# Performance work log

Hardware: AMD Instinct MI355X
Metric: run time of the kernel (lower is better)

Reference implementation:

```python
import jax, jax.numpy as jnp
import numpy as np

INPUT_SIZE = 512
N_THETA = 608  # backcast 512 + forecast 96
N_EXPERTS = 8
TOP_K = 2
LN_EPS = 1e-5


def setup_inputs() -> dict:
    key = jax.random.key(0)
    ks = jax.random.split(key, 5)
    B = 8192
    s = 0.02
    return {
        "insample_y": jax.random.normal(ks[0], (B, INPUT_SIZE), dtype=jnp.float32),
        "ln_gamma": jnp.ones((INPUT_SIZE,), dtype=jnp.float32),
        "ln_beta": jnp.zeros((INPUT_SIZE,), dtype=jnp.float32),
        "Wg": jax.random.normal(ks[1], (INPUT_SIZE, N_EXPERTS), dtype=jnp.float32) * s,
        "W0": jax.random.normal(ks[2], (N_EXPERTS, INPUT_SIZE, 512), dtype=jnp.float32) * s,
        "Wmid": jax.random.normal(ks[3], (3, N_EXPERTS, 512, 512), dtype=jnp.float32) * s,
        "Wout": jax.random.normal(ks[4], (N_EXPERTS, 512, N_THETA), dtype=jnp.float32) * s,
    }


def _layer_norm(x, gamma, beta):
    mu = jnp.mean(x, axis=-1, keepdims=True)
    var = jnp.mean(jnp.square(x - mu), axis=-1, keepdims=True)
    return (x - mu) * jax.lax.rsqrt(var + LN_EPS) * gamma + beta


def reference(insample_y, ln_gamma, ln_beta, Wg, W0, Wmid, Wout):
    x = insample_y  # [B, input_size]
    # Gate: LayerNorm -> Linear(no bias) -> top-k -> softmax over selected logits
    gate_logits = _layer_norm(x, ln_gamma, ln_beta) @ Wg            # [B, E]
    top_vals, top_idx = jax.lax.top_k(gate_logits, TOP_K)           # [B, k]
    gate_w = jax.nn.softmax(top_vals, axis=-1)                      # [B, k]

    # Experts (bias-free MLPs), evaluated densely for all experts
    z = jnp.einsum('bi,eih->beh', x, W0)                            # first linear, no activation
    for l in range(Wmid.shape[0]):
        z = jax.nn.relu(jnp.einsum('beh,eho->beo', z, Wmid[l]))
    theta_all = jnp.einsum('beh,eht->bet', z, Wout)                 # [B, E, n_theta]

    # Combine top-k expert outputs with gate weights
    theta_sel = jnp.take_along_axis(theta_all, top_idx[:, :, None], axis=1)  # [B, k, n_theta]
    theta = jnp.einsum('bk,bkt->bt', gate_w, theta_sel)             # [B, n_theta]

    # Identity basis: split theta into backcast / forecast
    backcast = theta[:, :INPUT_SIZE]
    forecast = theta[:, INPUT_SIZE:]
    return backcast, forecast
```

## Files before the change

kernel.cpp:

```cpp
#include <hip/hip_runtime.h>
#include <hip/hip_bf16.h>
#include <stdint.h>


#define B_ROWS 8192
#define I_DIM  512
#define H_DIM  512
#define E_NUM  8
#define T_DIM  608
#define T_PAD  640
#define CAP    2304
#define TPE    18
#define NT     144
#define NPAD   18432

typedef unsigned short ushort_t;
typedef __attribute__((ext_vector_type(8))) __bf16 bf16x8;
typedef __attribute__((ext_vector_type(8))) unsigned short ushort8;
typedef __attribute__((ext_vector_type(4))) float floatx4;

__device__ __forceinline__ void gload_lds16(const void* g, void* l) {
  __builtin_amdgcn_global_load_lds(
      (const __attribute__((address_space(1))) unsigned int*)g,
      (__attribute__((address_space(3))) unsigned int*)l, 16, 0, 0);
}

__device__ __forceinline__ ushort_t f2bf(float v) {
  __hip_bfloat16 h = __float2bfloat16(v);
  return __builtin_bit_cast(unsigned short, h);
}

__global__ __launch_bounds__(256) void gate_cast_k(
    const float* __restrict__ x, const float* __restrict__ gamma,
    const float* __restrict__ beta, const float* __restrict__ Wg,
    ushort_t* __restrict__ xb, int2* __restrict__ gidx, float2* __restrict__ gw)
{
  const int row  = (blockIdx.x * blockDim.x + threadIdx.x) >> 6;
  const int lane = threadIdx.x & 63;
  const float* xr = x + (size_t)row * I_DIM + lane * 8;
  float4 a = *(const float4*)(xr);
  float4 b = *(const float4*)(xr + 4);
  float xs[8] = {a.x, a.y, a.z, a.w, b.x, b.y, b.z, b.w};

  float s = 0.f;
#pragma unroll
  for (int j = 0; j < 8; ++j) s += xs[j];
#pragma unroll
  for (int off = 32; off; off >>= 1) s += __shfl_xor(s, off);
  const float mu = s * (1.0f / I_DIM);

  float vs = 0.f;
#pragma unroll
  for (int j = 0; j < 8; ++j) { float d = xs[j] - mu; vs += d * d; }
#pragma unroll
  for (int off = 32; off; off >>= 1) vs += __shfl_xor(vs, off);
  const float rstd = rsqrtf(vs * (1.0f / I_DIM) + 1e-5f);

  float lg[8] = {0.f, 0.f, 0.f, 0.f, 0.f, 0.f, 0.f, 0.f};
  const float* gmr = gamma + lane * 8;
  const float* btr = beta + lane * 8;
#pragma unroll
  for (int j = 0; j < 8; ++j) {
    const float y = (xs[j] - mu) * rstd * gmr[j] + btr[j];
    const float* wr = Wg + (size_t)(lane * 8 + j) * E_NUM;
#pragma unroll
    for (int e = 0; e < 8; ++e) lg[e] += y * wr[e];
  }
#pragma unroll
  for (int e = 0; e < 8; ++e)
#pragma unroll
    for (int off = 32; off; off >>= 1) lg[e] += __shfl_xor(lg[e], off);

  ushort8 o;
#pragma unroll
  for (int j = 0; j < 8; ++j) o[j] = f2bf(xs[j]);
  *(ushort8*)(xb + (size_t)row * I_DIM + lane * 8) = o;

  if (lane == 0) {
    int i0 = 0; float b0 = lg[0];
#pragma unroll
    for (int e = 1; e < 8; ++e) if (lg[e] > b0) { b0 = lg[e]; i0 = e; }
    int i1 = -1; float b1 = -3.4e38f;
#pragma unroll
    for (int e = 0; e < 8; ++e) if (e != i0 && lg[e] > b1) { b1 = lg[e]; i1 = e; }
    const float w0 = 1.0f / (1.0f + __expf(b1 - b0));
    gidx[row] = make_int2(i0, i1);
    gw[row] = make_float2(w0, 1.0f - w0);
  }
}

__global__ __launch_bounds__(256) void assign_k(
    const int2* __restrict__ gidx, const float2* __restrict__ gw,
    int* __restrict__ rowmap, float* __restrict__ wmap,
    int* __restrict__ cursor)
{
  __shared__ int lcnt[E_NUM];
  __shared__ int lbase[E_NUM];
  const int tid = threadIdx.x;
  const int row = blockIdx.x * 256 + tid;
  if (tid < E_NUM) lcnt[tid] = 0;
  __syncthreads();
  const int2 g = gidx[row];
  const float2 w = gw[row];
  const int r0 = atomicAdd(&lcnt[g.x], 1);
  const int r1 = atomicAdd(&lcnt[g.y], 1);
  __syncthreads();
  if (tid < E_NUM) lbase[tid] = atomicAdd(&cursor[tid], lcnt[tid]);
  __syncthreads();
  const int p0 = g.x * CAP + lbase[g.x] + r0;
  rowmap[p0] = row; wmap[p0] = w.x;
  const int p1 = g.y * CAP + lbase[g.y] + r1;
  rowmap[p1] = row; wmap[p1] = w.y;
}

__global__ __launch_bounds__(256) void transpose_cast_k(
    const float* __restrict__ src, ushort_t* __restrict__ dst,
    int R, int C, size_t srcBStr, size_t dstBStr)
{
  __shared__ float tile[32][33];
  src += (size_t)blockIdx.z * srcBStr;
  dst += (size_t)blockIdx.z * dstBStr;
  const int c0 = blockIdx.x * 32, r0 = blockIdx.y * 32;
  const int tx = threadIdx.x, ty = threadIdx.y;
#pragma unroll
  for (int i = 0; i < 4; ++i)
    tile[ty + i * 8][tx] = src[(size_t)(r0 + ty + i * 8) * C + c0 + tx];
  __syncthreads();
#pragma unroll
  for (int i = 0; i < 4; ++i) {
    const int c = c0 + ty + i * 8;
    if (c < C) dst[(size_t)c * R + r0 + tx] = f2bf(tile[tx][ty + i * 8]);
  }
}

template <bool GATHER, bool RELU, bool FINAL>
__global__ __launch_bounds__(256) void gemm_k(
    const ushort_t* __restrict__ A,
    const ushort_t* __restrict__ B,
    size_t bEStr,
    const int* __restrict__ rowmap, const float* __restrict__ wmap,
    const int* __restrict__ cursor,
    ushort_t* __restrict__ Z,
    float* __restrict__ out)
{
  constexpr int K = 512;
  __shared__ ushort_t lA[128 * 32];
  __shared__ ushort_t lB[128 * 32];
  __shared__ float wrow[128];
  __shared__ int rrow[128];

  const int t = blockIdx.x;
  const int e = t / TPE;
  if ((t - e * TPE) * 128 >= cursor[e]) return;
  const int zr0 = t * 128;
  const int bn0 = blockIdx.y * 128;

  const int tid = threadIdx.x, wid = tid >> 6, lane = tid & 63;
  const int sr = wid * 16 + (lane >> 2);
  const int sc = (lane & 3) * 8;

  const ushort_t* Bb = B + (size_t)e * bEStr + (size_t)bn0 * K;
  const ushort_t* gb = Bb + (size_t)sr * K + sc;
  const ushort_t *ga0, *ga1;
  if (GATHER) {
    ga0 = A + (size_t)rowmap[zr0 + sr] * K + sc;
    ga1 = A + (size_t)rowmap[zr0 + sr + 64] * K + sc;
  } else {
    ga0 = A + (size_t)(zr0 + sr) * K + sc;
    ga1 = ga0 + (size_t)64 * K;
  }
  ushort_t* la = lA + wid * 512;
  ushort_t* lb = lB + wid * 512;

  floatx4 acc[4][4] = {};
  const int wm = (wid >> 1) * 64, wn = (wid & 1) * 64;
  const int fr = lane & 15, q = lane >> 4;

  for (int k0 = 0; k0 < K; k0 += 32) {
    gload_lds16(ga0 + k0, la);
    gload_lds16(ga1 + k0, la + 64 * 32);
    gload_lds16(gb + k0, lb);
    gload_lds16(gb + (size_t)64 * K + k0, lb + 64 * 32);
    __syncthreads();

    bf16x8 af[4], bfr[4];
#pragma unroll
    for (int mi = 0; mi < 4; ++mi)
      af[mi] = *(const bf16x8*)(lA + (wm + mi * 16 + fr) * 32 + q * 8);
#pragma unroll
    for (int ni = 0; ni < 4; ++ni)
      bfr[ni] = *(const bf16x8*)(lB + (wn + ni * 16 + fr) * 32 + q * 8);
#pragma unroll
    for (int mi = 0; mi < 4; ++mi)
#pragma unroll
      for (int ni = 0; ni < 4; ++ni)
        acc[mi][ni] = __builtin_amdgcn_mfma_f32_16x16x32_bf16(
            af[mi], bfr[ni], acc[mi][ni], 0, 0, 0);
    __syncthreads();
  }

  if (!FINAL) {
    ushort_t* Zb = Z + (size_t)zr0 * H_DIM + bn0;
#pragma unroll
    for (int mi = 0; mi < 4; ++mi)
#pragma unroll
      for (int r = 0; r < 4; ++r) {
        const int row = wm + mi * 16 + q * 4 + r;
        ushort_t* zr = Zb + (size_t)row * H_DIM + wn + fr;
#pragma unroll
        for (int ni = 0; ni < 4; ++ni) {
          float v = acc[mi][ni][r];
          if (RELU) v = fmaxf(v, 0.0f);
          zr[ni * 16] = f2bf(v);
        }
      }
  } else {
    if (tid < 128) {
      wrow[tid] = wmap[zr0 + tid];
      rrow[tid] = rowmap[zr0 + tid];
    }
    __syncthreads();
#pragma unroll
    for (int mi = 0; mi < 4; ++mi)
#pragma unroll
      for (int r = 0; r < 4; ++r) {
        const int row = wm + mi * 16 + q * 4 + r;
        const float w = wrow[row];
        if (w != 0.0f) {
          const size_t orig = rrow[row];
#pragma unroll
          for (int ni = 0; ni < 4; ++ni) {
            const int col = bn0 + wn + ni * 16 + fr;
            if (col < T_DIM) {
              const float v = acc[mi][ni][r] * w;
              float* dst = (col < I_DIM)
                  ? out + orig * I_DIM + col
                  : out + (size_t)B_ROWS * I_DIM + orig * (T_DIM - I_DIM) +
                        (col - I_DIM);
              atomicAdd(dst, v);
            }
          }
        }
      }
  }
}

extern "C" void kernel_launch(void* const* d_in, const int* in_sizes, int n_in,
                              void* d_out, int out_size, void* d_ws,
                              size_t ws_size, hipStream_t stream) {
  const float* x     = (const float*)d_in[0];
  const float* gamma = (const float*)d_in[1];
  const float* beta  = (const float*)d_in[2];
  const float* Wg    = (const float*)d_in[3];
  const float* W0    = (const float*)d_in[4];
  const float* Wmid  = (const float*)d_in[5];
  const float* Wout  = (const float*)d_in[6];
  float* out = (float*)d_out;

  char* ws = (char*)d_ws;
  size_t off = 0;
  auto alloc = [&](size_t bytes) -> char* {
    char* p = ws + off;
    off += (bytes + 255) & ~(size_t)255;
    return p;
  };

  const size_t SQ = (size_t)H_DIM * H_DIM;
  ushort_t* xb    = (ushort_t*)alloc((size_t)B_ROWS * I_DIM * 2);
  ushort_t* W0t   = (ushort_t*)alloc((size_t)E_NUM * SQ * 2);
  ushort_t* Wmidt = (ushort_t*)alloc((size_t)3 * E_NUM * SQ * 2);
  ushort_t* Woutt = (ushort_t*)alloc((size_t)E_NUM * T_PAD * H_DIM * 2);
  int2*   gidx  = (int2*)alloc((size_t)B_ROWS * sizeof(int2));
  float2* gwv   = (float2*)alloc((size_t)B_ROWS * sizeof(float2));
  int*   rmap   = (int*)alloc(NPAD * sizeof(int));
  float* wmap   = (float*)alloc(NPAD * sizeof(float));
  int*   cursor = (int*)alloc(E_NUM * sizeof(int));
  ushort_t* z0 = (ushort_t*)alloc((size_t)NPAD * H_DIM * 2);
  ushort_t* z1 = (ushort_t*)alloc((size_t)NPAD * H_DIM * 2);

  hipMemsetAsync(d_out, 0, (size_t)out_size * sizeof(float), stream);
  hipMemsetAsync(rmap, 0, NPAD * sizeof(int), stream);
  hipMemsetAsync(wmap, 0, NPAD * sizeof(float), stream);
  hipMemsetAsync(cursor, 0, E_NUM * sizeof(int), stream);

  gate_cast_k<<<dim3(B_ROWS / 4), 256, 0, stream>>>(x, gamma, beta, Wg, xb,
                                                    gidx, gwv);
  transpose_cast_k<<<dim3(16, 16, 8), dim3(32, 8), 0, stream>>>(
      W0, W0t, 512, 512, SQ, SQ);
  transpose_cast_k<<<dim3(16, 16, 24), dim3(32, 8), 0, stream>>>(
      Wmid, Wmidt, 512, 512, SQ, SQ);
  transpose_cast_k<<<dim3(19, 16, 8), dim3(32, 8), 0, stream>>>(
      Wout, Woutt, 512, 608, (size_t)512 * 608, (size_t)T_PAD * 512);
  assign_k<<<dim3(B_ROWS / 256), 256, 0, stream>>>(gidx, gwv, rmap, wmap,
                                                   cursor);

  const dim3 gmid(NT, H_DIM / 128);
  const dim3 gfin(NT, T_PAD / 128);
  gemm_k<true, false, false><<<gmid, 256, 0, stream>>>(
      xb, W0t, SQ, rmap, wmap, cursor, z0, nullptr);
  gemm_k<false, true, false><<<gmid, 256, 0, stream>>>(
      z0, Wmidt + 0 * E_NUM * SQ, SQ, rmap, wmap, cursor, z1, nullptr);
  gemm_k<false, true, false><<<gmid, 256, 0, stream>>>(
      z1, Wmidt + 1 * E_NUM * SQ, SQ, rmap, wmap, cursor, z0, nullptr);
  gemm_k<false, true, false><<<gmid, 256, 0, stream>>>(
      z0, Wmidt + 2 * E_NUM * SQ, SQ, rmap, wmap, cursor, z1, nullptr);
  gemm_k<false, false, true><<<gfin, 256, 0, stream>>>(
      z1, Woutt, (size_t)T_PAD * H_DIM, rmap, wmap, cursor, nullptr, out);
}
```

Before: 256.0 us.

## Double-buffer LDS tiles with BK=64 and XOR swizzle in expert GEMM

Reworks the GEMM main loop to prefetch the next K-tile into a second LDS buffer while MFMAs run on the current one. It doubles the K tile to 64 to halve barrier count, and XOR-swizzles the LDS layout to avoid bank conflicts on fragment reads. It also sets launch bounds to two blocks per CU. LDS use grows to 64KB per block, which may limit occupancy, and there is one barrier per step with a waitcnt that could still serialize the loads.

After: 277.4 us. +8.4%, slower.

```diff
diff --git a/kernel.cpp b/kernel.cpp
--- a/kernel.cpp
+++ b/kernel.cpp
@@ -134,7 +134,7 @@
 }
 
 template <bool GATHER, bool RELU, bool FINAL>
-__global__ __launch_bounds__(256) void gemm_k(
+__global__ __launch_bounds__(256, 2) void gemm_k(
     const ushort_t* __restrict__ A,
     const ushort_t* __restrict__ B,
     size_t bEStr,
@@ -144,8 +144,10 @@
     float* __restrict__ out)
 {
   constexpr int K = 512;
-  __shared__ ushort_t lA[128 * 32];
-  __shared__ ushort_t lB[128 * 32];
+  constexpr int BK = 64;
+  constexpr int NSTEP = K / BK;
+  __shared__ ushort_t lA[2][128 * BK];
+  __shared__ ushort_t lB[2][128 * BK];
   __shared__ float wrow[128];
   __shared__ int rrow[128];
 
@@ -156,47 +158,79 @@
   const int bn0 = blockIdx.y * 128;
 
   const int tid = threadIdx.x, wid = tid >> 6, lane = tid & 63;
-  const int sr = wid * 16 + (lane >> 2);
-  const int sc = (lane & 3) * 8;
+  const int rl = lane >> 3;
+  const int kl = lane & 7;
+  const int ks = (kl ^ rl) * 8;
 
   const ushort_t* Bb = B + (size_t)e * bEStr + (size_t)bn0 * K;
-  const ushort_t* gb = Bb + (size_t)sr * K + sc;
-  const ushort_t *ga0, *ga1;
-  if (GATHER) {
-    ga0 = A + (size_t)rowmap[zr0 + sr] * K + sc;
-    ga1 = A + (size_t)rowmap[zr0 + sr + 64] * K + sc;
-  } else {
-    ga0 = A + (size_t)(zr0 + sr) * K + sc;
-    ga1 = ga0 + (size_t)64 * K;
-  }
-  ushort_t* la = lA + wid * 512;
-  ushort_t* lb = lB + wid * 512;
+  const ushort_t* gA[4];
+  const ushort_t* gB[4];
+#pragma unroll
+  for (int j = 0; j < 4; ++j) {
+    const int rloc = wid * 32 + j * 8 + rl;
+    int grow;
+    if (GATHER) grow = rowmap[zr0 + rloc];
+    else        grow = zr0 + rloc;
+    gA[j] = A + (size_t)grow * K + ks;
+    gB[j] = Bb + (size_t)rloc * K + ks;
+  }
+
+  auto stage = [&](int tt) {
+    ushort_t* da = lA[tt & 1];
+    ushort_t* db = lB[tt & 1];
+    const int k0 = tt * BK;
+#pragma unroll
+    for (int j = 0; j < 4; ++j) {
+      gload_lds16(gA[j] + k0, da + (wid * 32 + j * 8) * BK);
+      gload_lds16(gB[j] + k0, db + (wid * 32 + j * 8) * BK);
+    }
+  };
 
   floatx4 acc[4][4] = {};
   const int wm = (wid >> 1) * 64, wn = (wid & 1) * 64;
   const int fr = lane & 15, q = lane >> 4;
 
-  for (int k0 = 0; k0 < K; k0 += 32) {
-    gload_lds16(ga0 + k0, la);
-    gload_lds16(ga1 + k0, la + 64 * 32);
-    gload_lds16(gb + k0, lb);
-    gload_lds16(gb + (size_t)64 * K + k0, lb + 64 * 32);
-    __syncthreads();
-
-    bf16x8 af[4], bfr[4];
-#pragma unroll
-    for (int mi = 0; mi < 4; ++mi)
-      af[mi] = *(const bf16x8*)(lA + (wm + mi * 16 + fr) * 32 + q * 8);
-#pragma unroll
-    for (int ni = 0; ni < 4; ++ni)
-      bfr[ni] = *(const bf16x8*)(lB + (wn + ni * 16 + fr) * 32 + q * 8);
-#pragma unroll
-    for (int mi = 0; mi < 4; ++mi)
-#pragma unroll
-      for (int ni = 0; ni < 4; ++ni)
-        acc[mi][ni] = __builtin_amdgcn_mfma_f32_16x16x32_bf16(
-            af[mi], bfr[ni], acc[mi][ni], 0, 0, 0);
-    __syncthreads();
+  stage(0);
+  asm volatile("s_waitcnt vmcnt(0)" ::: "memory");
+  __builtin_amdgcn_s_barrier();
+
+#pragma unroll
+  for (int step = 0; step < NSTEP; ++step) {
+    const int cur = step & 1;
+    if (step < NSTEP - 1) stage(step + 1);
+
+    bf16x8 af[4][2], bfr[4][2];
+    const char* bA = (const char*)lA[cur];
+    const char* bB = (const char*)lB[cur];
+#pragma unroll
+    for (int mi = 0; mi < 4; ++mi) {
+      const int row = wm + mi * 16 + fr;
+      const int rb = row * 128, rx = (row & 7) << 4;
+#pragma unroll
+      for (int kk = 0; kk < 2; ++kk)
+        af[mi][kk] = *(const bf16x8*)(bA + ((rb + kk * 64 + q * 16) ^ rx));
+    }
+#pragma unroll
+    for (int ni = 0; ni < 4; ++ni) {
+      const int row = wn + ni * 16 + fr;
+      const int rb = row * 128, rx = (row & 7) << 4;
+#pragma unroll
+      for (int kk = 0; kk < 2; ++kk)
+        bfr[ni][kk] = *(const bf16x8*)(bB + ((rb + kk * 64 + q * 16) ^ rx));
+    }
+#pragma unroll
+    for (int kk = 0; kk < 2; ++kk)
+#pragma unroll
+      for (int mi = 0; mi < 4; ++mi)
+#pragma unroll
+        for (int ni = 0; ni < 4; ++ni)
+          acc[mi][ni] = __builtin_amdgcn_mfma_f32_16x16x32_bf16(
+              af[mi][kk], bfr[ni][kk], acc[mi][ni], 0, 0, 0);
+
+    if (step < NSTEP - 1) {
+      asm volatile("s_waitcnt vmcnt(0)" ::: "memory");
+      __builtin_amdgcn_s_barrier();
+    }
   }
 
   if (!FINAL) {
```

## Fuse all five expert MLP layers into one kernel keeping activations in LDS

Applied to the files above, without the earlier changes.

Replaces the five per-layer grouped GEMM launches with a single kernel. Each block owns 64 routed rows of one expert and keeps that activation tile in a 64 KB XOR-swizzled LDS buffer across all layers, while weight fragments are streamed straight from global memory into registers with double buffering. This removes the global round-trips of the intermediate z buffers and four launch boundaries. In exchange every block re-reads the full expert weights from global/L2, and occupancy is limited by the large LDS footprint and register use.

Result: slower. 415.4 us (+62.3%).

```diff
diff --git a/kernel.cpp b/kernel.cpp
--- a/kernel.cpp
+++ b/kernel.cpp
@@ -10,8 +10,8 @@
 #define T_DIM  608
 #define T_PAD  640
 #define CAP    2304
-#define TPE    18
-#define NT     144
+#define TPW    36
+#define NB     288
 #define NPAD   18432
 
 typedef unsigned short ushort_t;
@@ -133,116 +133,164 @@
   }
 }
 
-template <bool GATHER, bool RELU, bool FINAL>
-__global__ __launch_bounds__(256) void gemm_k(
-    const ushort_t* __restrict__ A,
-    const ushort_t* __restrict__ B,
-    size_t bEStr,
-    const int* __restrict__ rowmap, const float* __restrict__ wmap,
-    const int* __restrict__ cursor,
-    ushort_t* __restrict__ Z,
-    float* __restrict__ out)
-{
-  constexpr int K = 512;
-  __shared__ ushort_t lA[128 * 32];
-  __shared__ ushort_t lB[128 * 32];
-  __shared__ float wrow[128];
-  __shared__ int rrow[128];
-
-  const int t = blockIdx.x;
-  const int e = t / TPE;
-  if ((t - e * TPE) * 128 >= cursor[e]) return;
-  const int zr0 = t * 128;
-  const int bn0 = blockIdx.y * 128;
-
-  const int tid = threadIdx.x, wid = tid >> 6, lane = tid & 63;
-  const int sr = wid * 16 + (lane >> 2);
-  const int sc = (lane & 3) * 8;
-
-  const ushort_t* Bb = B + (size_t)e * bEStr + (size_t)bn0 * K;
-  const ushort_t* gb = Bb + (size_t)sr * K + sc;
-  const ushort_t *ga0, *ga1;
-  if (GATHER) {
-    ga0 = A + (size_t)rowmap[zr0 + sr] * K + sc;
-    ga1 = A + (size_t)rowmap[zr0 + sr + 64] * K + sc;
-  } else {
-    ga0 = A + (size_t)(zr0 + sr) * K + sc;
-    ga1 = ga0 + (size_t)64 * K;
-  }
-  ushort_t* la = lA + wid * 512;
-  ushort_t* lb = lB + wid * 512;
-
-  floatx4 acc[4][4] = {};
-  const int wm = (wid >> 1) * 64, wn = (wid & 1) * 64;
-  const int fr = lane & 15, q = lane >> 4;
-
-  for (int k0 = 0; k0 < K; k0 += 32) {
-    gload_lds16(ga0 + k0, la);
-    gload_lds16(ga1 + k0, la + 64 * 32);
-    gload_lds16(gb + k0, lb);
-    gload_lds16(gb + (size_t)64 * K + k0, lb + 64 * 32);
-    __syncthreads();
-
-    bf16x8 af[4], bfr[4];
-#pragma unroll
-    for (int mi = 0; mi < 4; ++mi)
-      af[mi] = *(const bf16x8*)(lA + (wm + mi * 16 + fr) * 32 + q * 8);
-#pragma unroll
-    for (int ni = 0; ni < 4; ++ni)
-      bfr[ni] = *(const bf16x8*)(lB + (wn + ni * 16 + fr) * 32 + q * 8);
-#pragma unroll
-    for (int mi = 0; mi < 4; ++mi)
-#pragma unroll
-      for (int ni = 0; ni < 4; ++ni)
-        acc[mi][ni] = __builtin_amdgcn_mfma_f32_16x16x32_bf16(
-            af[mi], bfr[ni], acc[mi][ni], 0, 0, 0);
-    __syncthreads();
-  }
-
-  if (!FINAL) {
-    ushort_t* Zb = Z + (size_t)zr0 * H_DIM + bn0;
-#pragma unroll
-    for (int mi = 0; mi < 4; ++mi)
-#pragma unroll
-      for (int r = 0; r < 4; ++r) {
-        const int row = wm + mi * 16 + q * 4 + r;
-        ushort_t* zr = Zb + (size_t)row * H_DIM + wn + fr;
-#pragma unroll
-        for (int ni = 0; ni < 4; ++ni) {
-          float v = acc[mi][ni][r];
-          if (RELU) v = fmaxf(v, 0.0f);
-          zr[ni * 16] = f2bf(v);
-        }
+
+template <int NF, bool RELU>
+__device__ __forceinline__ void layer_z(
+    const ushort_t* __restrict__ Wt, char* __restrict__ z,
+    int n0, int fr, int q)
+{
+  const ushort_t* wb[NF];
+#pragma unroll
+  for (int nf = 0; nf < NF; ++nf)
+    wb[nf] = Wt + (size_t)(n0 + nf * 16 + fr) * 512 + q * 8;
+
+  bf16x8 Wr[2][NF];
+#pragma unroll
+  for (int nf = 0; nf < NF; ++nf) Wr[0][nf] = *(const bf16x8*)(wb[nf]);
+
+  floatx4 acc[NF][4] = {};
+#pragma unroll
+  for (int s = 0; s < 16; ++s) {
+    if (s < 15) {
+#pragma unroll
+      for (int nf = 0; nf < NF; ++nf)
+        Wr[(s + 1) & 1][nf] = *(const bf16x8*)(wb[nf] + (s + 1) * 32);
+    }
+#pragma unroll
+    for (int mf = 0; mf < 4; ++mf) {
+      const int m = mf * 16 + fr;
+      const bf16x8 zf = *(const bf16x8*)(
+          z + m * 1024 + ((s * 64 + q * 16) ^ ((m & 7) << 4)));
+#pragma unroll
+      for (int nf = 0; nf < NF; ++nf)
+        acc[nf][mf] = __builtin_amdgcn_mfma_f32_16x16x32_bf16(
+            Wr[s & 1][nf], zf, acc[nf][mf], 0, 0, 0);
+    }
+  }
+
+  ushort4 st[NF][4];
+#pragma unroll
+  for (int nf = 0; nf < NF; ++nf)
+#pragma unroll
+    for (int mf = 0; mf < 4; ++mf) {
+      float v0 = acc[nf][mf][0], v1 = acc[nf][mf][1];
+      float v2 = acc[nf][mf][2], v3 = acc[nf][mf][3];
+      if (RELU) {
+        v0 = fmaxf(v0, 0.f); v1 = fmaxf(v1, 0.f);
+        v2 = fmaxf(v2, 0.f); v3 = fmaxf(v3, 0.f);
       }
-  } else {
-    if (tid < 128) {
-      wrow[tid] = wmap[zr0 + tid];
-      rrow[tid] = rowmap[zr0 + tid];
-    }
-    __syncthreads();
-#pragma unroll
-    for (int mi = 0; mi < 4; ++mi)
-#pragma unroll
-      for (int r = 0; r < 4; ++r) {
-        const int row = wm + mi * 16 + q * 4 + r;
-        const float w = wrow[row];
-        if (w != 0.0f) {
-          const size_t orig = rrow[row];
-#pragma unroll
-          for (int ni = 0; ni < 4; ++ni) {
-            const int col = bn0 + wn + ni * 16 + fr;
-            if (col < T_DIM) {
-              const float v = acc[mi][ni][r] * w;
-              float* dst = (col < I_DIM)
-                  ? out + orig * I_DIM + col
-                  : out + (size_t)B_ROWS * I_DIM + orig * (T_DIM - I_DIM) +
-                        (col - I_DIM);
-              atomicAdd(dst, v);
-            }
+      st[nf][mf] = make_ushort4(f2bf(v0), f2bf(v1), f2bf(v2), f2bf(v3));
+    }
+
+  __syncthreads();
+#pragma unroll
+  for (int nf = 0; nf < NF; ++nf) {
+    const int nbyte = (n0 + nf * 16 + q * 4) * 2;
+#pragma unroll
+    for (int mf = 0; mf < 4; ++mf) {
+      const int m = mf * 16 + fr;
+      *(ushort4*)(z + m * 1024 + (nbyte ^ ((m & 7) << 4))) = st[nf][mf];
+    }
+  }
+  __syncthreads();
+}
+
+template <int NF>
+__device__ __forceinline__ void layer_final(
+    const ushort_t* __restrict__ Wt, const char* __restrict__ z,
+    int n0, int zr0, const int* __restrict__ rowmap,
+    const float* __restrict__ wmap, float* __restrict__ out,
+    int fr, int q)
+{
+  const ushort_t* wb[NF];
+#pragma unroll
+  for (int nf = 0; nf < NF; ++nf)
+    wb[nf] = Wt + (size_t)(n0 + nf * 16 + fr) * 512 + q * 8;
+
+  bf16x8 Wr[2][NF];
+#pragma unroll
+  for (int nf = 0; nf < NF; ++nf) Wr[0][nf] = *(const bf16x8*)(wb[nf]);
+
+  floatx4 acc[NF][4] = {};
+#pragma unroll
+  for (int s = 0; s < 16; ++s) {
+    if (s < 15) {
+#pragma unroll
+      for (int nf = 0; nf < NF; ++nf)
+        Wr[(s + 1) & 1][nf] = *(const bf16x8*)(wb[nf] + (s + 1) * 32);
+    }
+#pragma unroll
+    for (int mf = 0; mf < 4; ++mf) {
+      const int m = mf * 16 + fr;
+      const bf16x8 zf = *(const bf16x8*)(
+          z + m * 1024 + ((s * 64 + q * 16) ^ ((m & 7) << 4)));
+#pragma unroll
+      for (int nf = 0; nf < NF; ++nf)
+        acc[nf][mf] = __builtin_amdgcn_mfma_f32_16x16x32_bf16(
+            Wr[s & 1][nf], zf, acc[nf][mf], 0, 0, 0);
+    }
+  }
+
+#pragma unroll
+  for (int mf = 0; mf < 4; ++mf) {
+    const int m = mf * 16 + fr;
+    const float wgt = wmap[zr0 + m];
+    if (wgt != 0.0f) {
+      const size_t orig = rowmap[zr0 + m];
+#pragma unroll
+      for (int nf = 0; nf < NF; ++nf)
+#pragma unroll
+        for (int r = 0; r < 4; ++r) {
+          const int col = n0 + nf * 16 + q * 4 + r;
+          if (col < T_DIM) {
+            const float v = acc[nf][mf][r] * wgt;
+            float* dst = (col < I_DIM)
+                ? out + orig * I_DIM + col
+                : out + (size_t)B_ROWS * I_DIM + orig * (T_DIM - I_DIM) +
+                      (col - I_DIM);
+            atomicAdd(dst, v);
           }
         }
-      }
-  }
+    }
+  }
+}
+
+__global__ __launch_bounds__(256, 2) void moe_chain_k(
+    const ushort_t* __restrict__ xb, const ushort_t* __restrict__ W0t,
+    const ushort_t* __restrict__ Wmidt, const ushort_t* __restrict__ Woutt,
+    const int* __restrict__ rowmap, const float* __restrict__ wmap,
+    const int* __restrict__ cursor, float* __restrict__ out)
+{
+  __shared__ char zb[64 * 1024];
+
+  const int b = blockIdx.x;
+  const int e = b & 7;
+  const int lt = b >> 3;
+  if (lt * 64 >= cursor[e]) return;
+  const int zr0 = e * CAP + lt * 64;
+
+  const int tid = threadIdx.x, wid = tid >> 6, lane = tid & 63;
+  const int fr = lane & 15, q = lane >> 4;
+
+#pragma unroll
+  for (int i = 0; i < 16; ++i) {
+    const int r = wid * 16 + i;
+    const ushort_t* src = xb + (size_t)rowmap[zr0 + r] * 512 +
+                          ((lane ^ (r & 7)) * 8);
+    gload_lds16(src, zb + r * 1024);
+  }
+  __syncthreads();
+
+  const size_t SQ = (size_t)512 * 512;
+  const int n0 = wid * 128;
+  layer_z<8, false>(W0t + (size_t)e * SQ, zb, n0, fr, q);
+  layer_z<8, true>(Wmidt + (size_t)(0 * E_NUM + e) * SQ, zb, n0, fr, q);
+  layer_z<8, true>(Wmidt + (size_t)(1 * E_NUM + e) * SQ, zb, n0, fr, q);
+  layer_z<8, true>(Wmidt + (size_t)(2 * E_NUM + e) * SQ, zb, n0, fr, q);
+
+  const ushort_t* We = Woutt + (size_t)e * T_PAD * 512;
+  layer_final<5>(We, zb, wid * 160,      zr0, rowmap, wmap, out, fr, q);
+  layer_final<5>(We, zb, wid * 160 + 80, zr0, rowmap, wmap, out, fr, q);
 }
 
 extern "C" void kernel_launch(void* const* d_in, const int* in_sizes, int n_in,
@@ -275,8 +323,6 @@
   int*   rmap   = (int*)alloc(NPAD * sizeof(int));
   float* wmap   = (float*)alloc(NPAD * sizeof(float));
   int*   cursor = (int*)alloc(E_NUM * sizeof(int));
-  ushort_t* z0 = (ushort_t*)alloc((size_t)NPAD * H_DIM * 2);
-  ushort_t* z1 = (ushort_t*)alloc((size_t)NPAD * H_DIM * 2);
 
   hipMemsetAsync(d_out, 0, (size_t)out_size * sizeof(float), stream);
   hipMemsetAsync(rmap, 0, NPAD * sizeof(int), stream);
@@ -294,16 +340,6 @@
   assign_k<<<dim3(B_ROWS / 256), 256, 0, stream>>>(gidx, gwv, rmap, wmap,
                                                    cursor);
 
-  const dim3 gmid(NT, H_DIM / 128);
-  const dim3 gfin(NT, T_PAD / 128);
-  gemm_k<true, false, false><<<gmid, 256, 0, stream>>>(
-      xb, W0t, SQ, rmap, wmap, cursor, z0, nullptr);
-  gemm_k<false, true, false><<<gmid, 256, 0, stream>>>(
-      z0, Wmidt + 0 * E_NUM * SQ, SQ, rmap, wmap, cursor, z1, nullptr);
-  gemm_k<false, true, false><<<gmid, 256, 0, stream>>>(
-      z1, Wmidt + 1 * E_NUM * SQ, SQ, rmap, wmap, cursor, z0, nullptr);
-  gemm_k<false, true, false><<<gmid, 256, 0, stream>>>(
-      z0, Wmidt + 2 * E_NUM * SQ, SQ, rmap, wmap, cursor, z1, nullptr);
-  gemm_k<false, false, true><<<gfin, 256, 0, stream>>>(
-      z1, Woutt, (size_t)T_PAD * H_DIM, rmap, wmap, cursor, nullptr, out);
-}
+  moe_chain_k<<<dim3(NB), 256, 0, stream>>>(xb, W0t, Wmidt, Woutt, rmap, wmap,
+                                            cursor, out);
+}
```

## Keep full-K expert weight slab in LDS and stream A from global

Applied to the files above, without the earlier changes.

The expert GEMM kernel is restructured so each block preloads a 64-column, full-K (512) slab of the expert weight matrix into 64KB of XOR-swizzled LDS once. Each wave then computes 64 rows against it, loading A fragments straight from global memory with no per-k-step barriers. The grid becomes (expert, 256-row chunk, 64-column tile), with early exit per wave on the expert's row count, and launch bounds request 2 blocks per CU. This removes the per-iteration syncthreads and LDS staging of A. In exchange, A loads are uncoalesced per-lane global reads that may raise latency, and the large LDS footprint limits occupancy.

After: 322.1 us. +25.8%, slower.

```diff
diff --git a/kernel.cpp b/kernel.cpp
--- a/kernel.cpp
+++ b/kernel.cpp
@@ -10,8 +10,6 @@
 #define T_DIM  608
 #define T_PAD  640
 #define CAP    2304
-#define TPE    18
-#define NT     144
 #define NPAD   18432
 
 typedef unsigned short ushort_t;
@@ -134,7 +132,7 @@
 }
 
 template <bool GATHER, bool RELU, bool FINAL>
-__global__ __launch_bounds__(256) void gemm_k(
+__global__ __launch_bounds__(256, 2) void gemm_k(
     const ushort_t* __restrict__ A,
     const ushort_t* __restrict__ B,
     size_t bEStr,
@@ -143,96 +141,87 @@
     ushort_t* __restrict__ Z,
     float* __restrict__ out)
 {
-  constexpr int K = 512;
-  __shared__ ushort_t lA[128 * 32];
-  __shared__ ushort_t lB[128 * 32];
-  __shared__ float wrow[128];
-  __shared__ int rrow[128];
-
-  const int t = blockIdx.x;
-  const int e = t / TPE;
-  if ((t - e * TPE) * 128 >= cursor[e]) return;
-  const int zr0 = t * 128;
-  const int bn0 = blockIdx.y * 128;
+  __shared__ char lB[64 * 1024];
+
+  const int e  = blockIdx.x;
+  const int m9 = blockIdx.y;
+  const int n0 = blockIdx.z * 64;
+  const int cnt = cursor[e];
+  if (m9 * 256 >= cnt) return;
+  const int zr0 = e * CAP;
 
   const int tid = threadIdx.x, wid = tid >> 6, lane = tid & 63;
-  const int sr = wid * 16 + (lane >> 2);
-  const int sc = (lane & 3) * 8;
-
-  const ushort_t* Bb = B + (size_t)e * bEStr + (size_t)bn0 * K;
-  const ushort_t* gb = Bb + (size_t)sr * K + sc;
-  const ushort_t *ga0, *ga1;
-  if (GATHER) {
-    ga0 = A + (size_t)rowmap[zr0 + sr] * K + sc;
-    ga1 = A + (size_t)rowmap[zr0 + sr + 64] * K + sc;
-  } else {
-    ga0 = A + (size_t)(zr0 + sr) * K + sc;
-    ga1 = ga0 + (size_t)64 * K;
-  }
-  ushort_t* la = lA + wid * 512;
-  ushort_t* lb = lB + wid * 512;
+  const int fr = lane & 15, q = lane >> 4;
+
+  const ushort_t* Bb = B + (size_t)e * bEStr + (size_t)n0 * 512;
+#pragma unroll
+  for (int j = 0; j < 16; ++j) {
+    const int col = wid * 16 + j;
+    const int sb = (lane * 16) ^ ((col & 7) << 4);
+    gload_lds16((const char*)(Bb + (size_t)col * 512) + sb,
+                lB + col * 1024 + lane * 16);
+  }
+  __syncthreads();
+
+  const int r0 = m9 * 256 + wid * 64;
+  if (r0 >= cnt) return;
+
+  const ushort_t* ga[4];
+#pragma unroll
+  for (int s2 = 0; s2 < 4; ++s2) {
+    const int slot = zr0 + r0 + s2 * 16 + fr;
+    const int ar = GATHER ? rowmap[slot] : slot;
+    ga[s2] = A + (size_t)ar * 512 + q * 8;
+  }
 
   floatx4 acc[4][4] = {};
-  const int wm = (wid >> 1) * 64, wn = (wid & 1) * 64;
-  const int fr = lane & 15, q = lane >> 4;
-
-  for (int k0 = 0; k0 < K; k0 += 32) {
-    gload_lds16(ga0 + k0, la);
-    gload_lds16(ga1 + k0, la + 64 * 32);
-    gload_lds16(gb + k0, lb);
-    gload_lds16(gb + (size_t)64 * K + k0, lb + 64 * 32);
-    __syncthreads();
-
-    bf16x8 af[4], bfr[4];
-#pragma unroll
-    for (int mi = 0; mi < 4; ++mi)
-      af[mi] = *(const bf16x8*)(lA + (wm + mi * 16 + fr) * 32 + q * 8);
-#pragma unroll
-    for (int ni = 0; ni < 4; ++ni)
-      bfr[ni] = *(const bf16x8*)(lB + (wn + ni * 16 + fr) * 32 + q * 8);
-#pragma unroll
-    for (int mi = 0; mi < 4; ++mi)
+#pragma unroll
+  for (int c = 0; c < 16; ++c) {
+    bf16x8 bfv[4];
+#pragma unroll
+    for (int ni = 0; ni < 4; ++ni) {
+      const int col = ni * 16 + fr;
+      bfv[ni] = *(const bf16x8*)(
+          lB + col * 1024 + ((c * 64 + q * 16) ^ ((col & 7) << 4)));
+    }
+#pragma unroll
+    for (int s2 = 0; s2 < 4; ++s2) {
+      const bf16x8 af = *(const bf16x8*)(ga[s2] + c * 32);
 #pragma unroll
       for (int ni = 0; ni < 4; ++ni)
-        acc[mi][ni] = __builtin_amdgcn_mfma_f32_16x16x32_bf16(
-            af[mi], bfr[ni], acc[mi][ni], 0, 0, 0);
-    __syncthreads();
+        acc[s2][ni] = __builtin_amdgcn_mfma_f32_16x16x32_bf16(
+            af, bfv[ni], acc[s2][ni], 0, 0, 0);
+    }
   }
 
   if (!FINAL) {
-    ushort_t* Zb = Z + (size_t)zr0 * H_DIM + bn0;
-#pragma unroll
-    for (int mi = 0; mi < 4; ++mi)
+#pragma unroll
+    for (int s2 = 0; s2 < 4; ++s2)
 #pragma unroll
       for (int r = 0; r < 4; ++r) {
-        const int row = wm + mi * 16 + q * 4 + r;
-        ushort_t* zr = Zb + (size_t)row * H_DIM + wn + fr;
+        const int slot = zr0 + r0 + s2 * 16 + q * 4 + r;
+        ushort_t* zrp = Z + (size_t)slot * H_DIM + n0 + fr;
 #pragma unroll
         for (int ni = 0; ni < 4; ++ni) {
-          float v = acc[mi][ni][r];
+          float v = acc[s2][ni][r];
           if (RELU) v = fmaxf(v, 0.0f);
-          zr[ni * 16] = f2bf(v);
+          zrp[ni * 16] = f2bf(v);
         }
       }
   } else {
-    if (tid < 128) {
-      wrow[tid] = wmap[zr0 + tid];
-      rrow[tid] = rowmap[zr0 + tid];
-    }
-    __syncthreads();
-#pragma unroll
-    for (int mi = 0; mi < 4; ++mi)
+#pragma unroll
+    for (int s2 = 0; s2 < 4; ++s2)
 #pragma unroll
       for (int r = 0; r < 4; ++r) {
-        const int row = wm + mi * 16 + q * 4 + r;
-        const float w = wrow[row];
+        const int slot = zr0 + r0 + s2 * 16 + q * 4 + r;
+        const float w = wmap[slot];
         if (w != 0.0f) {
-          const size_t orig = rrow[row];
+          const size_t orig = rowmap[slot];
 #pragma unroll
           for (int ni = 0; ni < 4; ++ni) {
-            const int col = bn0 + wn + ni * 16 + fr;
+            const int col = n0 + ni * 16 + fr;
             if (col < T_DIM) {
-              const float v = acc[mi][ni][r] * w;
+              const float v = acc[s2][ni][r] * w;
               float* dst = (col < I_DIM)
                   ? out + orig * I_DIM + col
                   : out + (size_t)B_ROWS * I_DIM + orig * (T_DIM - I_DIM) +
@@ -294,8 +283,8 @@
   assign_k<<<dim3(B_ROWS / 256), 256, 0, stream>>>(gidx, gwv, rmap, wmap,
                                                    cursor);
 
-  const dim3 gmid(NT, H_DIM / 128);
-  const dim3 gfin(NT, T_PAD / 128);
+  const dim3 gmid(E_NUM, CAP / 256, H_DIM / 64);
+  const dim3 gfin(E_NUM, CAP / 256, T_PAD / 64);
   gemm_k<true, false, false><<<gmid, 256, 0, stream>>>(
       xb, W0t, SQ, rmap, wmap, cursor, z0, nullptr);
   gemm_k<false, true, false><<<gmid, 256, 0, stream>>>(
```
